# Optimization experiments

Hardware: AMD Instinct MI355X
Metric: run time of the kernel (lower is better)

## Reference

```python
import jax, jax.numpy as jnp
import numpy as np

N_NODES = 20000
N_EDGES = 100000
MUL = 128          # channels per irrep
R = 8              # radial (edge scalar) features
H = 64             # radial MLP hidden width
SILU_NORM = 1.6790390826      # e3nn normalize2mom constant for SiLU
INV_SQRT3 = 1.0 / np.sqrt(3.0)   # wigner-3j values for l<=1 paths
PW_0E = np.sqrt(0.5)   # e3nn path weight: out dim 1, fan-in 2 paths
PW_1O = np.sqrt(1.5)   # e3nn path weight: out dim 3, fan-in 2 paths


def setup_inputs() -> dict:
    key = jax.random.key(0)
    ks = jax.random.split(key, 12)
    return dict(
        node_feats=jax.random.normal(ks[0], (N_NODES, 4 * MUL), jnp.float32),
        edge_attrs=jax.random.normal(ks[1], (N_EDGES, 4), jnp.float32),   # SH: 1x0e+1x1o
        edge_feats=jax.random.normal(ks[2], (N_EDGES, R), jnp.float32),
        edge_index=jax.random.randint(ks[3], (2, N_EDGES), 0, N_NODES),
        W_up_s=jax.random.normal(ks[4], (MUL, MUL), jnp.float32),
        W_up_v=jax.random.normal(ks[5], (MUL, MUL), jnp.float32),
        mlp_w0=jax.random.normal(ks[6], (R, H), jnp.float32),
        mlp_w1=jax.random.normal(ks[7], (H, H), jnp.float32),
        mlp_w2=jax.random.normal(ks[8], (H, H), jnp.float32),
        mlp_w3=jax.random.normal(ks[9], (H, 4 * MUL), jnp.float32),
        W_out_s=jax.random.normal(ks[10], (2 * MUL, MUL), jnp.float32),
        W_out_v=jax.random.normal(ks[11], (2 * MUL, MUL), jnp.float32),
    )


def reference(node_feats, edge_attrs, edge_feats, edge_index,
              W_up_s, W_up_v, mlp_w0, mlp_w1, mlp_w2, mlp_w3,
              W_out_s, W_out_v):
    sender = edge_index[0]
    # split node feats into irrep blocks: 128x0e then 128x1o (channel-major [u, m])
    s = node_feats[:, :MUL]                       # [N, 128]
    v = node_feats[:, MUL:].reshape(-1, MUL, 3)   # [N, 128, 3]
    # linear_up: per-irrep e3nn Linear, fan_in-normalized
    s = (s @ W_up_s) / np.sqrt(MUL)
    v = jnp.einsum('nui,uw->nwi', v, W_up_v) / np.sqrt(MUL)
    # radial MLP -> per-edge tensor-product weights (e3nn FullyConnectedNet)
    act = lambda x: jax.nn.silu(x) * SILU_NORM
    h = act(edge_feats @ (mlp_w0 / np.sqrt(R)))
    h = act(h @ (mlp_w1 / np.sqrt(H)))
    h = act(h @ (mlp_w2 / np.sqrt(H)))
    tpw = h @ (mlp_w3 / np.sqrt(H))               # [E, 4*128]
    w00, w01, w10, w11 = jnp.split(tpw, 4, axis=1)  # instruction order of weight_numel
    # gather sender node features per edge
    ss = s[sender]                                # [E, 128]
    vs = v[sender]                                # [E, 128, 3]
    sh0 = edge_attrs[:, :1]                       # [E, 1]  scalar SH
    sh1 = edge_attrs[:, 1:]                       # [E, 3]  l=1 SH
    # uvu CG tensor product paths (l<=1 wigner-3j)
    a0 = PW_0E * w00 * ss * sh0                                   # 0e x 0e -> 0e
    a1 = (PW_1O * INV_SQRT3) * (w01 * ss)[:, :, None] * sh1[:, None, :]   # 0e x 1o -> 1o
    b1 = (PW_1O * INV_SQRT3) * (w10 * sh0)[:, :, None] * vs              # 1o x 0e -> 1o
    b0 = (PW_0E * INV_SQRT3) * w11 * jnp.einsum('eui,ei->eu', vs, sh1)   # 1o x 1o -> 0e
    # irreps_mid sorted+simplified: 256x0e + 256x1o
    mid_s = jnp.concatenate([a0, b0], axis=1)     # [E, 256]
    mid_v = jnp.concatenate([a1, b1], axis=1)     # [E, 256, 3]
    # final per-irrep linear to target 128x0e + 128x1o
    out_s = (mid_s @ W_out_s) / np.sqrt(2 * MUL)
    out_v = jnp.einsum('eui,uw->ewi', mid_v, W_out_v) / np.sqrt(2 * MUL)
    return jnp.concatenate([out_s, out_v.reshape(out_v.shape[0], 3 * MUL)], axis=1)
```

## Files before the change

kernel.cpp:

```cpp
#include <hip/hip_runtime.h>
#include <stdint.h>

#define N_NODES 20000
#define N_EDGES 100000

typedef __bf16 bf16;
typedef bf16  bf16x8 __attribute__((ext_vector_type(8)));
typedef float f32x4  __attribute__((ext_vector_type(4)));

__device__ __forceinline__ f32x4 mfma16(bf16x8 a, bf16x8 b, f32x4 c) {
  return __builtin_amdgcn_mfma_f32_16x16x32_bf16(a, b, c, 0, 0, 0);
}

__device__ __forceinline__ float silu_(float y) {
  return y / (1.0f + __expf(-y));
}

#define OFF_W0T   0u
#define OFF_W1T   4096u
#define OFF_W2T   12288u
#define OFF_W3T   20480u
#define OFF_WOS   86016u
#define OFF_WOV   151552u
#define OFF_WST   217088u
#define OFF_WVT   249856u
#define OFF_SUP   282624u
#define OFF_VUP   5402624u

__global__ __launch_bounds__(256) void k0_prep(
    const float* __restrict__ wus, const float* __restrict__ wuv,
    const float* __restrict__ w0,  const float* __restrict__ w1,
    const float* __restrict__ w2,  const float* __restrict__ w3,
    const float* __restrict__ wos_g, const float* __restrict__ wov_g,
    char* __restrict__ ws) {
  const int idx = blockIdx.x * 256 + threadIdx.x;
  bf16* W0T = (bf16*)(ws + OFF_W0T);
  bf16* W1T = (bf16*)(ws + OFF_W1T);
  bf16* W2T = (bf16*)(ws + OFF_W2T);
  bf16* W3T = (bf16*)(ws + OFF_W3T);
  bf16* WOS = (bf16*)(ws + OFF_WOS);
  bf16* WOV = (bf16*)(ws + OFF_WOV);
  bf16* WST = (bf16*)(ws + OFF_WST);
  bf16* WVT = (bf16*)(ws + OFF_WVT);

  const float cS   = 0.08838834764831845f;
  const float c0   = 0.35355339059327373f;
  const float c12  = 1.6790390826f / 8.0f;
  const float cosA = 0.04419417382415922f;
  const float cosB = 0.025515518153991442f;
  const float cov  = 0.04419417382415922f;

  if (idx < 16384) {
    int w = idx >> 7, u = idx & 127;
    WST[idx] = (bf16)(wus[u * 128 + w] * cS);
    WVT[idx] = (bf16)(wuv[u * 128 + w] * cS);
  }
  if (idx < 2048) {
    int h = idx >> 5, r = idx & 31;
    W0T[idx] = (bf16)((r < 8) ? w0[r * 64 + h] * c0 : 0.0f);
  }
  if (idx < 4096) {
    int h = idx >> 6, k = idx & 63;
    W1T[idx] = (bf16)(w1[k * 64 + h] * c12);
    W2T[idx] = (bf16)(w2[k * 64 + h] * c12);
  }
  {
    int j = idx >> 6, k = idx & 63;
    W3T[idx] = (bf16)(w3[k * 512 + j] * c12);
    int w = idx >> 8, u = idx & 255;
    WOS[idx] = (bf16)(wos_g[u * 128 + w] * ((u < 128) ? cosA : cosB));
    WOV[idx] = (bf16)(wov_g[u * 128 + w] * cov);
  }
}

__global__ __launch_bounds__(256) void k1_nodeup(const float* __restrict__ nf,
                                                 char* __restrict__ ws) {
  __shared__ bf16 At[64 * 136];
  const int n0 = blockIdx.x * 64;
  const int sid = blockIdx.y;
  const int t = threadIdx.x;

  #pragma unroll
  for (int p = 0; p < 32; p++) {
    int idx = t + p * 256;
    int r = idx >> 7, k = idx & 127;
    int node = n0 + r;
    float v = 0.0f;
    if (node < N_NODES)
      v = (sid == 0) ? nf[node * 512 + k]
                     : nf[node * 512 + 128 + 3 * k + (sid - 1)];
    At[r * 136 + k] = (bf16)v;
  }
  __syncthreads();

  const bf16* BT = (const bf16*)(ws + ((sid == 0) ? OFF_WST : OFF_WVT));
  const int lane = t & 63, wv = t >> 6;
  const int m = lane & 15, q = lane >> 4;
  const int m0 = wv * 16;

  const f32x4 z = {0.f, 0.f, 0.f, 0.f};
  f32x4 acc[8] = {z, z, z, z, z, z, z, z};
  #pragma unroll
  for (int kk = 0; kk < 128; kk += 32) {
    bf16x8 af = *(const bf16x8*)&At[(m0 + m) * 136 + kk + q * 8];
    #pragma unroll
    for (int nt = 0; nt < 8; nt++) {
      bf16x8 bfr = *(const bf16x8*)&BT[(nt * 16 + m) * 128 + kk + q * 8];
      acc[nt] = mfma16(af, bfr, acc[nt]);
    }
  }

  bf16* sup = (bf16*)(ws + OFF_SUP);
  bf16* vup = (bf16*)(ws + OFF_VUP);
  #pragma unroll
  for (int nt = 0; nt < 8; nt++) {
    int col = nt * 16 + m;
    #pragma unroll
    for (int r = 0; r < 4; r++) {
      int row = m0 + q * 4 + r;
      int node = n0 + row;
      if (node < N_NODES) {
        if (sid == 0) sup[node * 128 + col] = (bf16)acc[nt][r];
        else          vup[node * 384 + (sid - 1) * 128 + col] = (bf16)acc[nt][r];
      }
    }
  }
}

__global__ __launch_bounds__(256) void k2_mlp(const float* __restrict__ efeat,
                                              const char* __restrict__ ws,
                                              float* __restrict__ tpw) {
  __shared__ bf16 A0[64 * 40];
  __shared__ bf16 hA[64 * 72];
  __shared__ bf16 hB[64 * 72];
  const int e0 = blockIdx.x * 64;
  const int t = threadIdx.x;
  const int lane = t & 63, wv = t >> 6;
  const int m = lane & 15, q = lane >> 4;
  const int m0 = wv * 16;
  const f32x4 z = {0.f, 0.f, 0.f, 0.f};

  #pragma unroll
  for (int p = 0; p < 8; p++) {
    int idx = t + p * 256;
    int r = idx >> 5, k = idx & 31;
    int e = e0 + r;
    float v = (k < 8 && e < N_EDGES) ? efeat[e * 8 + k] : 0.0f;
    A0[r * 40 + k] = (bf16)v;
  }
  __syncthreads();

  const bf16* W0T = (const bf16*)(ws + OFF_W0T);
  const bf16* W1T = (const bf16*)(ws + OFF_W1T);
  const bf16* W2T = (const bf16*)(ws + OFF_W2T);
  const bf16* W3T = (const bf16*)(ws + OFF_W3T);

  {
    f32x4 acc[4] = {z, z, z, z};
    bf16x8 af = *(const bf16x8*)&A0[(m0 + m) * 40 + q * 8];
    #pragma unroll
    for (int nt = 0; nt < 4; nt++) {
      bf16x8 bfr = *(const bf16x8*)&W0T[(nt * 16 + m) * 32 + q * 8];
      acc[nt] = mfma16(af, bfr, acc[nt]);
    }
    #pragma unroll
    for (int nt = 0; nt < 4; nt++)
      #pragma unroll
      for (int r = 0; r < 4; r++)
        hA[(m0 + q * 4 + r) * 72 + nt * 16 + m] = (bf16)silu_(acc[nt][r]);
  }
  __syncthreads();

  {
    f32x4 acc[4] = {z, z, z, z};
    #pragma unroll
    for (int kk = 0; kk < 64; kk += 32) {
      bf16x8 af = *(const bf16x8*)&hA[(m0 + m) * 72 + kk + q * 8];
      #pragma unroll
      for (int nt = 0; nt < 4; nt++) {
        bf16x8 bfr = *(const bf16x8*)&W1T[(nt * 16 + m) * 64 + kk + q * 8];
        acc[nt] = mfma16(af, bfr, acc[nt]);
      }
    }
    #pragma unroll
    for (int nt = 0; nt < 4; nt++)
      #pragma unroll
      for (int r = 0; r < 4; r++)
        hB[(m0 + q * 4 + r) * 72 + nt * 16 + m] = (bf16)silu_(acc[nt][r]);
  }
  __syncthreads();

  {
    f32x4 acc[4] = {z, z, z, z};
    #pragma unroll
    for (int kk = 0; kk < 64; kk += 32) {
      bf16x8 af = *(const bf16x8*)&hB[(m0 + m) * 72 + kk + q * 8];
      #pragma unroll
      for (int nt = 0; nt < 4; nt++) {
        bf16x8 bfr = *(const bf16x8*)&W2T[(nt * 16 + m) * 64 + kk + q * 8];
        acc[nt] = mfma16(af, bfr, acc[nt]);
      }
    }
    __syncthreads();
    #pragma unroll
    for (int nt = 0; nt < 4; nt++)
      #pragma unroll
      for (int r = 0; r < 4; r++)
        hA[(m0 + q * 4 + r) * 72 + nt * 16 + m] = (bf16)silu_(acc[nt][r]);
  }
  __syncthreads();

  {
    bf16x8 af0 = *(const bf16x8*)&hA[(m0 + m) * 72 + 0  + q * 8];
    bf16x8 af1 = *(const bf16x8*)&hA[(m0 + m) * 72 + 32 + q * 8];
    const int row0 = m0 + q * 4;
    #pragma unroll 4
    for (int nt = 0; nt < 32; nt++) {
      f32x4 acc = z;
      bf16x8 b0 = *(const bf16x8*)&W3T[(nt * 16 + m) * 64 + q * 8];
      bf16x8 b1 = *(const bf16x8*)&W3T[(nt * 16 + m) * 64 + 32 + q * 8];
      acc = mfma16(af0, b0, acc);
      acc = mfma16(af1, b1, acc);
      int col = nt * 16 + m;
      #pragma unroll
      for (int r = 0; r < 4; r++) {
        int e = e0 + row0 + r;
        if (e < N_EDGES) tpw[e * 512 + col] = acc[r];
      }
    }
  }
}

__global__ __launch_bounds__(256) void k3_tp_out(const float* __restrict__ attrs,
                                                 const int* __restrict__ sender,
                                                 const char* __restrict__ ws,
                                                 float* out) {
  __shared__ bf16 A[128 * 72];
  __shared__ int   sLDS[32];
  __shared__ float aLDS[128];
  const int e0 = blockIdx.x * 32;
  const int t = threadIdx.x;
  if (t < 32) sLDS[t] = sender[e0 + t];
  if (t < 128) aLDS[t] = attrs[e0 * 4 + t];
  __syncthreads();

  const bf16* sup = (const bf16*)(ws + OFF_SUP);
  const bf16* vup = (const bf16*)(ws + OFF_VUP);
  const int lane = t & 63, wv = t >> 6;
  const int m = lane & 15, q = lane >> 4;
  const bf16* WB = (const bf16*)(ws + ((wv == 0) ? OFF_WOS : OFF_WOV));

  const int srow = t >> 1;
  const int kh = (t & 1) * 32;
  const bool isS = (srow < 32);
  const int ii = isS ? 0 : ((srow - 32) >> 5);
  const int eL = isS ? srow : ((srow - 32) & 31);
  const int eG = e0 + eL;
  const int se = sLDS[eL];
  const float s0  = aLDS[eL * 4 + 0];
  const float s1x = aLDS[eL * 4 + 1];
  const float s1y = aLDS[eL * 4 + 2];
  const float s1z = aLDS[eL * 4 + 3];
  const float s1i = (ii == 0) ? s1x : ((ii == 1) ? s1y : s1z);
  const float* tpr = out + (size_t)eG * 512;
  const bf16* supR = sup + se * 128;
  const bf16* vupR = vup + se * 384;

  const f32x4 z = {0.f, 0.f, 0.f, 0.f};
  f32x4 acc0[8] = {z, z, z, z, z, z, z, z};
  f32x4 acc1[8] = {z, z, z, z, z, z, z, z};

  for (int kc = 0; kc < 4; kc++) {
    if (kc) __syncthreads();
    if (kc < 2) {
      const int ub = kc * 64 + kh;
      if (isS) {
        #pragma unroll 8
        for (int j = 0; j < 32; j++) {
          int u = ub + j;
          A[srow * 72 + kh + j] = (bf16)(tpr[u] * (float)supR[u] * s0);
        }
      } else {
        #pragma unroll 8
        for (int j = 0; j < 32; j++) {
          int u = ub + j;
          A[srow * 72 + kh + j] = (bf16)(tpr[128 + u] * (float)supR[u] * s1i);
        }
      }
    } else {
      const int ub = (kc - 2) * 64 + kh;
      if (isS) {
        #pragma unroll 8
        for (int j = 0; j < 32; j++) {
          int up = ub + j;
          float dv = (float)vupR[up] * s1x + (float)vupR[128 + up] * s1y +
                     (float)vupR[256 + up] * s1z;
          A[srow * 72 + kh + j] = (bf16)(tpr[384 + up] * dv);
        }
      } else {
        #pragma unroll 8
        for (int j = 0; j < 32; j++) {
          int up = ub + j;
          A[srow * 72 + kh + j] =
              (bf16)(tpr[256 + up] * s0 * (float)vupR[ii * 128 + up]);
        }
      }
    }
    __syncthreads();

    const int kb = kc * 64;
    #pragma unroll
    for (int kk = 0; kk < 64; kk += 32) {
      bf16x8 af0 = *(const bf16x8*)&A[(wv * 32 + m) * 72 + kk + q * 8];
      bf16x8 af1 = *(const bf16x8*)&A[(wv * 32 + 16 + m) * 72 + kk + q * 8];
      #pragma unroll
      for (int nt = 0; nt < 8; nt++) {
        bf16x8 bfr = *(const bf16x8*)&WB[(nt * 16 + m) * 256 + kb + kk + q * 8];
        acc0[nt] = mfma16(af0, bfr, acc0[nt]);
        acc1[nt] = mfma16(af1, bfr, acc1[nt]);
      }
    }
  }

  #pragma unroll
  for (int b = 0; b < 2; b++) {
    const f32x4* accp = b ? acc1 : acc0;
    int rb = wv * 32 + b * 16 + q * 4;
    #pragma unroll
    for (int nt = 0; nt < 8; nt++) {
      int col = nt * 16 + m;
      #pragma unroll
      for (int r = 0; r < 4; r++) {
        int row = rb + r;
        float v = accp[nt][r];
        if (wv == 0) {
          out[(size_t)(e0 + row) * 512 + col] = v;
        } else {
          int i2 = (row - 32) >> 5, eL2 = (row - 32) & 31;
          out[(size_t)(e0 + eL2) * 512 + 128 + 3 * col + i2] = v;
        }
      }
    }
  }
}

extern "C" void kernel_launch(void* const* d_in, const int* in_sizes, int n_in,
                              void* d_out, int out_size, void* d_ws, size_t ws_size,
                              hipStream_t stream) {
  const float* node_feats = (const float*)d_in[0];
  const float* edge_attrs = (const float*)d_in[1];
  const float* edge_feats = (const float*)d_in[2];
  const int*   edge_index = (const int*)d_in[3];
  const float* W_up_s = (const float*)d_in[4];
  const float* W_up_v = (const float*)d_in[5];
  const float* w0 = (const float*)d_in[6];
  const float* w1 = (const float*)d_in[7];
  const float* w2 = (const float*)d_in[8];
  const float* w3 = (const float*)d_in[9];
  const float* Wos = (const float*)d_in[10];
  const float* Wov = (const float*)d_in[11];
  float* out = (float*)d_out;
  char* ws = (char*)d_ws;

  k0_prep<<<dim3(128), dim3(256), 0, stream>>>(W_up_s, W_up_v, w0, w1, w2, w3,
                                               Wos, Wov, ws);
  k1_nodeup<<<dim3(313, 4), dim3(256), 0, stream>>>(node_feats, ws);
  k2_mlp<<<dim3(1563), dim3(256), 0, stream>>>(edge_feats, ws, out);
  k3_tp_out<<<dim3(3125), dim3(256), 0, stream>>>(edge_attrs, edge_index, ws, out);
}
```

Baseline: 542.7 us.

## Fuse radial MLP into tensor-product kernel, keep TP weights in LDS

Merges the radial MLP kernel into the tensor-product/output kernel, so the per-edge 512-wide TP weights stay in shared memory as bf16 instead of being written to and re-read from the output buffer in fp32. The node-up kernel now reads node features once with float4 loads and deinterleaves all four irrep components in one block, rather than launching four strided passes. The TP gather loops are vectorized to 8-wide bf16 loads. The cost is more LDS per block (about 52KB), which limits occupancy, and the MLP work is now split across 32-edge blocks with extra barriers.

```diff
diff --git a/kernel.cpp b/kernel.cpp
--- a/kernel.cpp
+++ b/kernel.cpp
@@ -73,80 +73,107 @@
   }
 }
 
-__global__ __launch_bounds__(256) void k1_nodeup(const float* __restrict__ nf,
-                                                 char* __restrict__ ws) {
-  __shared__ bf16 At[64 * 136];
-  const int n0 = blockIdx.x * 64;
-  const int sid = blockIdx.y;
+__global__ __launch_bounds__(256, 4) void k1_nodeup(const float* __restrict__ nf,
+                                                    char* __restrict__ ws) {
+  __shared__ __align__(16) bf16 tiles[4][32 * 136];
+  const int n0 = blockIdx.x * 32;
   const int t = threadIdx.x;
 
   #pragma unroll
-  for (int p = 0; p < 32; p++) {
-    int idx = t + p * 256;
-    int r = idx >> 7, k = idx & 127;
-    int node = n0 + r;
-    float v = 0.0f;
-    if (node < N_NODES)
-      v = (sid == 0) ? nf[node * 512 + k]
-                     : nf[node * 512 + 128 + 3 * k + (sid - 1)];
-    At[r * 136 + k] = (bf16)v;
-  }
-  __syncthreads();
-
-  const bf16* BT = (const bf16*)(ws + ((sid == 0) ? OFF_WST : OFF_WVT));
-  const int lane = t & 63, wv = t >> 6;
+  for (int p = 0; p < 16; p++) {
+    int idx = p * 256 + t;
+    int r = idx >> 7, c4 = idx & 127;
+    const float4 f = *(const float4*)&nf[(size_t)(n0 + r) * 512 + c4 * 4];
+    float vals[4] = {f.x, f.y, f.z, f.w};
+    #pragma unroll
+    for (int e2 = 0; e2 < 4; e2++) {
+      int g = c4 * 4 + e2;
+      if (g < 128) {
+        tiles[0][r * 136 + g] = (bf16)vals[e2];
+      } else {
+        int gg = g - 128;
+        int u = gg / 3, i = gg - 3 * u;
+        tiles[1 + i][r * 136 + u] = (bf16)vals[e2];
+      }
+    }
+  }
+  __syncthreads();
+
+  const int wv = t >> 6, lane = t & 63;
   const int m = lane & 15, q = lane >> 4;
-  const int m0 = wv * 16;
+  const bf16* BT = (const bf16*)(ws + ((wv == 0) ? OFF_WST : OFF_WVT));
+  const bf16* At = tiles[wv];
 
   const f32x4 z = {0.f, 0.f, 0.f, 0.f};
-  f32x4 acc[8] = {z, z, z, z, z, z, z, z};
+  f32x4 acc[2][8] = {{z, z, z, z, z, z, z, z}, {z, z, z, z, z, z, z, z}};
   #pragma unroll
   for (int kk = 0; kk < 128; kk += 32) {
-    bf16x8 af = *(const bf16x8*)&At[(m0 + m) * 136 + kk + q * 8];
+    bf16x8 af0 = *(const bf16x8*)&At[m * 136 + kk + q * 8];
+    bf16x8 af1 = *(const bf16x8*)&At[(16 + m) * 136 + kk + q * 8];
     #pragma unroll
     for (int nt = 0; nt < 8; nt++) {
       bf16x8 bfr = *(const bf16x8*)&BT[(nt * 16 + m) * 128 + kk + q * 8];
-      acc[nt] = mfma16(af, bfr, acc[nt]);
+      acc[0][nt] = mfma16(af0, bfr, acc[0][nt]);
+      acc[1][nt] = mfma16(af1, bfr, acc[1][nt]);
     }
   }
 
   bf16* sup = (bf16*)(ws + OFF_SUP);
   bf16* vup = (bf16*)(ws + OFF_VUP);
   #pragma unroll
-  for (int nt = 0; nt < 8; nt++) {
-    int col = nt * 16 + m;
-    #pragma unroll
-    for (int r = 0; r < 4; r++) {
-      int row = m0 + q * 4 + r;
-      int node = n0 + row;
-      if (node < N_NODES) {
-        if (sid == 0) sup[node * 128 + col] = (bf16)acc[nt][r];
-        else          vup[node * 384 + (sid - 1) * 128 + col] = (bf16)acc[nt][r];
-      }
-    }
-  }
-}
-
-__global__ __launch_bounds__(256) void k2_mlp(const float* __restrict__ efeat,
-                                              const char* __restrict__ ws,
-                                              float* __restrict__ tpw) {
-  __shared__ bf16 A0[64 * 40];
-  __shared__ bf16 hA[64 * 72];
-  __shared__ bf16 hB[64 * 72];
-  const int e0 = blockIdx.x * 64;
+  for (int rt = 0; rt < 2; rt++) {
+    #pragma unroll
+    for (int nt = 0; nt < 8; nt++) {
+      int col = nt * 16 + m;
+      #pragma unroll
+      for (int r = 0; r < 4; r++) {
+        int node = n0 + rt * 16 + q * 4 + r;
+        if (wv == 0) sup[node * 128 + col] = (bf16)acc[rt][nt][r];
+        else         vup[node * 384 + (wv - 1) * 128 + col] = (bf16)acc[rt][nt][r];
+      }
+    }
+  }
+}
+
+#define SM_TPW 0
+#define SM_A   33280
+#define SM_A0  33280
+#define SM_H0  (33280 + 2560)
+#define SM_H1  (33280 + 7168)
+#define SM_SND 51712
+#define SM_ATT 51840
+#define TPW_LD 520
+
+__global__ __launch_bounds__(256, 3) void k23_fused(
+    const float* __restrict__ efeat, const float* __restrict__ attrs,
+    const int* __restrict__ sender, const char* __restrict__ ws,
+    float* __restrict__ out) {
+  __shared__ __align__(16) char smem[52352];
+  bf16* tpwL = (bf16*)(smem + SM_TPW);
+  bf16* A    = (bf16*)(smem + SM_A);
+  bf16* A0e  = (bf16*)(smem + SM_A0);
+  bf16* h0   = (bf16*)(smem + SM_H0);
+  bf16* h1   = (bf16*)(smem + SM_H1);
+  int*  sLDS = (int*)(smem + SM_SND);
+  float* aLDS = (float*)(smem + SM_ATT);
+
+  const int e0 = blockIdx.x * 32;
   const int t = threadIdx.x;
-  const int lane = t & 63, wv = t >> 6;
+  const int wv = t >> 6, lane = t & 63;
   const int m = lane & 15, q = lane >> 4;
-  const int m0 = wv * 16;
   const f32x4 z = {0.f, 0.f, 0.f, 0.f};
 
-  #pragma unroll
-  for (int p = 0; p < 8; p++) {
-    int idx = t + p * 256;
-    int r = idx >> 5, k = idx & 31;
-    int e = e0 + r;
-    float v = (k < 8 && e < N_EDGES) ? efeat[e * 8 + k] : 0.0f;
-    A0[r * 40 + k] = (bf16)v;
+  {
+    int r = t >> 3, k = t & 7;
+    A0e[r * 40 + k] = (bf16)efeat[(e0 + r) * 8 + k];
+    #pragma unroll
+    for (int pp = 0; pp < 3; pp++) {
+      int pidx = t * 3 + pp;
+      int r2 = pidx / 24, k2 = 8 + pidx % 24;
+      A0e[r2 * 40 + k2] = (bf16)0.0f;
+    }
+    if (t < 32) sLDS[t] = sender[e0 + t];
+    if (t < 128) aLDS[t] = attrs[e0 * 4 + t];
   }
   __syncthreads();
 
@@ -155,99 +182,89 @@
   const bf16* W2T = (const bf16*)(ws + OFF_W2T);
   const bf16* W3T = (const bf16*)(ws + OFF_W3T);
 
-  {
-    f32x4 acc[4] = {z, z, z, z};
-    bf16x8 af = *(const bf16x8*)&A0[(m0 + m) * 40 + q * 8];
-    #pragma unroll
-    for (int nt = 0; nt < 4; nt++) {
-      bf16x8 bfr = *(const bf16x8*)&W0T[(nt * 16 + m) * 32 + q * 8];
-      acc[nt] = mfma16(af, bfr, acc[nt]);
-    }
-    #pragma unroll
-    for (int nt = 0; nt < 4; nt++)
+  const int rt = wv & 1, nh = wv >> 1;
+
+  {
+    f32x4 acc[2] = {z, z};
+    bf16x8 af = *(const bf16x8*)&A0e[(rt * 16 + m) * 40 + q * 8];
+    #pragma unroll
+    for (int ntl = 0; ntl < 2; ntl++) {
+      int ntg = nh * 2 + ntl;
+      bf16x8 bfr = *(const bf16x8*)&W0T[(ntg * 16 + m) * 32 + q * 8];
+      acc[ntl] = mfma16(af, bfr, acc[ntl]);
+    }
+    __syncthreads();
+    #pragma unroll
+    for (int ntl = 0; ntl < 2; ntl++)
       #pragma unroll
       for (int r = 0; r < 4; r++)
-        hA[(m0 + q * 4 + r) * 72 + nt * 16 + m] = (bf16)silu_(acc[nt][r]);
-  }
-  __syncthreads();
-
-  {
-    f32x4 acc[4] = {z, z, z, z};
+        h0[(rt * 16 + q * 4 + r) * 72 + (nh * 2 + ntl) * 16 + m] = (bf16)silu_(acc[ntl][r]);
+  }
+  __syncthreads();
+
+  {
+    f32x4 acc[2] = {z, z};
     #pragma unroll
     for (int kk = 0; kk < 64; kk += 32) {
-      bf16x8 af = *(const bf16x8*)&hA[(m0 + m) * 72 + kk + q * 8];
-      #pragma unroll
-      for (int nt = 0; nt < 4; nt++) {
-        bf16x8 bfr = *(const bf16x8*)&W1T[(nt * 16 + m) * 64 + kk + q * 8];
-        acc[nt] = mfma16(af, bfr, acc[nt]);
-      }
-    }
-    #pragma unroll
-    for (int nt = 0; nt < 4; nt++)
+      bf16x8 af = *(const bf16x8*)&h0[(rt * 16 + m) * 72 + kk + q * 8];
+      #pragma unroll
+      for (int ntl = 0; ntl < 2; ntl++) {
+        int ntg = nh * 2 + ntl;
+        bf16x8 bfr = *(const bf16x8*)&W1T[(ntg * 16 + m) * 64 + kk + q * 8];
+        acc[ntl] = mfma16(af, bfr, acc[ntl]);
+      }
+    }
+    __syncthreads();
+    #pragma unroll
+    for (int ntl = 0; ntl < 2; ntl++)
       #pragma unroll
       for (int r = 0; r < 4; r++)
-        hB[(m0 + q * 4 + r) * 72 + nt * 16 + m] = (bf16)silu_(acc[nt][r]);
-  }
-  __syncthreads();
-
-  {
-    f32x4 acc[4] = {z, z, z, z};
+        h1[(rt * 16 + q * 4 + r) * 72 + (nh * 2 + ntl) * 16 + m] = (bf16)silu_(acc[ntl][r]);
+  }
+  __syncthreads();
+
+  {
+    f32x4 acc[2] = {z, z};
     #pragma unroll
     for (int kk = 0; kk < 64; kk += 32) {
-      bf16x8 af = *(const bf16x8*)&hB[(m0 + m) * 72 + kk + q * 8];
-      #pragma unroll
-      for (int nt = 0; nt < 4; nt++) {
-        bf16x8 bfr = *(const bf16x8*)&W2T[(nt * 16 + m) * 64 + kk + q * 8];
-        acc[nt] = mfma16(af, bfr, acc[nt]);
+      bf16x8 af = *(const bf16x8*)&h1[(rt * 16 + m) * 72 + kk + q * 8];
+      #pragma unroll
+      for (int ntl = 0; ntl < 2; ntl++) {
+        int ntg = nh * 2 + ntl;
+        bf16x8 bfr = *(const bf16x8*)&W2T[(ntg * 16 + m) * 64 + kk + q * 8];
+        acc[ntl] = mfma16(af, bfr, acc[ntl]);
       }
     }
     __syncthreads();
     #pragma unroll
-    for (int nt = 0; nt < 4; nt++)
+    for (int ntl = 0; ntl < 2; ntl++)
       #pragma unroll
       for (int r = 0; r < 4; r++)
-        hA[(m0 + q * 4 + r) * 72 + nt * 16 + m] = (bf16)silu_(acc[nt][r]);
-  }
-  __syncthreads();
-
-  {
-    bf16x8 af0 = *(const bf16x8*)&hA[(m0 + m) * 72 + 0  + q * 8];
-    bf16x8 af1 = *(const bf16x8*)&hA[(m0 + m) * 72 + 32 + q * 8];
-    const int row0 = m0 + q * 4;
+        h0[(rt * 16 + q * 4 + r) * 72 + (nh * 2 + ntl) * 16 + m] = (bf16)silu_(acc[ntl][r]);
+  }
+  __syncthreads();
+
+  {
+    bf16x8 af0 = *(const bf16x8*)&h0[(rt * 16 + m) * 72 + 0  + q * 8];
+    bf16x8 af1 = *(const bf16x8*)&h0[(rt * 16 + m) * 72 + 32 + q * 8];
     #pragma unroll 4
-    for (int nt = 0; nt < 32; nt++) {
+    for (int i = 0; i < 16; i++) {
+      int ntg = nh * 16 + i;
       f32x4 acc = z;
-      bf16x8 b0 = *(const bf16x8*)&W3T[(nt * 16 + m) * 64 + q * 8];
-      bf16x8 b1 = *(const bf16x8*)&W3T[(nt * 16 + m) * 64 + 32 + q * 8];
+      bf16x8 b0 = *(const bf16x8*)&W3T[(ntg * 16 + m) * 64 + q * 8];
+      bf16x8 b1 = *(const bf16x8*)&W3T[(ntg * 16 + m) * 64 + 32 + q * 8];
       acc = mfma16(af0, b0, acc);
       acc = mfma16(af1, b1, acc);
-      int col = nt * 16 + m;
-      #pragma unroll
-      for (int r = 0; r < 4; r++) {
-        int e = e0 + row0 + r;
-        if (e < N_EDGES) tpw[e * 512 + col] = acc[r];
-      }
-    }
-  }
-}
-
-__global__ __launch_bounds__(256) void k3_tp_out(const float* __restrict__ attrs,
-                                                 const int* __restrict__ sender,
-                                                 const char* __restrict__ ws,
-                                                 float* out) {
-  __shared__ bf16 A[128 * 72];
-  __shared__ int   sLDS[32];
-  __shared__ float aLDS[128];
-  const int e0 = blockIdx.x * 32;
-  const int t = threadIdx.x;
-  if (t < 32) sLDS[t] = sender[e0 + t];
-  if (t < 128) aLDS[t] = attrs[e0 * 4 + t];
+      int col = ntg * 16 + m;
+      #pragma unroll
+      for (int r = 0; r < 4; r++)
+        tpwL[(rt * 16 + q * 4 + r) * TPW_LD + col] = (bf16)acc[r];
+    }
+  }
   __syncthreads();
 
   const bf16* sup = (const bf16*)(ws + OFF_SUP);
   const bf16* vup = (const bf16*)(ws + OFF_VUP);
-  const int lane = t & 63, wv = t >> 6;
-  const int m = lane & 15, q = lane >> 4;
   const bf16* WB = (const bf16*)(ws + ((wv == 0) ? OFF_WOS : OFF_WOV));
 
   const int srow = t >> 1;
@@ -255,18 +272,16 @@
   const bool isS = (srow < 32);
   const int ii = isS ? 0 : ((srow - 32) >> 5);
   const int eL = isS ? srow : ((srow - 32) & 31);
-  const int eG = e0 + eL;
   const int se = sLDS[eL];
   const float s0  = aLDS[eL * 4 + 0];
   const float s1x = aLDS[eL * 4 + 1];
   const float s1y = aLDS[eL * 4 + 2];
   const float s1z = aLDS[eL * 4 + 3];
   const float s1i = (ii == 0) ? s1x : ((ii == 1) ? s1y : s1z);
-  const float* tpr = out + (size_t)eG * 512;
+  const bf16* tpr = tpwL + eL * TPW_LD;
   const bf16* supR = sup + se * 128;
   const bf16* vupR = vup + se * 384;
 
-  const f32x4 z = {0.f, 0.f, 0.f, 0.f};
   f32x4 acc0[8] = {z, z, z, z, z, z, z, z};
   f32x4 acc1[8] = {z, z, z, z, z, z, z, z};
 
@@ -275,34 +290,55 @@
     if (kc < 2) {
       const int ub = kc * 64 + kh;
       if (isS) {
-        #pragma unroll 8
-        for (int j = 0; j < 32; j++) {
-          int u = ub + j;
-          A[srow * 72 + kh + j] = (bf16)(tpr[u] * (float)supR[u] * s0);
+        #pragma unroll
+        for (int j0 = 0; j0 < 32; j0 += 8) {
+          bf16x8 tv = *(const bf16x8*)&tpr[ub + j0];
+          bf16x8 sv = *(const bf16x8*)&supR[ub + j0];
+          bf16x8 o;
+          #pragma unroll
+          for (int e = 0; e < 8; e++)
+            o[e] = (bf16)((float)tv[e] * (float)sv[e] * s0);
+          *(bf16x8*)&A[srow * 72 + kh + j0] = o;
         }
       } else {
-        #pragma unroll 8
-        for (int j = 0; j < 32; j++) {
-          int u = ub + j;
-          A[srow * 72 + kh + j] = (bf16)(tpr[128 + u] * (float)supR[u] * s1i);
+        #pragma unroll
+        for (int j0 = 0; j0 < 32; j0 += 8) {
+          bf16x8 tv = *(const bf16x8*)&tpr[128 + ub + j0];
+          bf16x8 sv = *(const bf16x8*)&supR[ub + j0];
+          bf16x8 o;
+          #pragma unroll
+          for (int e = 0; e < 8; e++)
+            o[e] = (bf16)((float)tv[e] * (float)sv[e] * s1i);
+          *(bf16x8*)&A[srow * 72 + kh + j0] = o;
         }
       }
     } else {
       const int ub = (kc - 2) * 64 + kh;
       if (isS) {
-        #pragma unroll 8
-        for (int j = 0; j < 32; j++) {
-          int up = ub + j;
-          float dv = (float)vupR[up] * s1x + (float)vupR[128 + up] * s1y +
-                     (float)vupR[256 + up] * s1z;
-          A[srow * 72 + kh + j] = (bf16)(tpr[384 + up] * dv);
+        #pragma unroll
+        for (int j0 = 0; j0 < 32; j0 += 8) {
+          bf16x8 tv = *(const bf16x8*)&tpr[384 + ub + j0];
+          bf16x8 vx = *(const bf16x8*)&vupR[ub + j0];
+          bf16x8 vy = *(const bf16x8*)&vupR[128 + ub + j0];
+          bf16x8 vz = *(const bf16x8*)&vupR[256 + ub + j0];
+          bf16x8 o;
+          #pragma unroll
+          for (int e = 0; e < 8; e++) {
+            float dv = (float)vx[e] * s1x + (float)vy[e] * s1y + (float)vz[e] * s1z;
+            o[e] = (bf16)((float)tv[e] * dv);
+          }
+          *(bf16x8*)&A[srow * 72 + kh + j0] = o;
         }
       } else {
-        #pragma unroll 8
-        for (int j = 0; j < 32; j++) {
-          int up = ub + j;
-          A[srow * 72 + kh + j] =
-              (bf16)(tpr[256 + up] * s0 * (float)vupR[ii * 128 + up]);
+        #pragma unroll
+        for (int j0 = 0; j0 < 32; j0 += 8) {
+          bf16x8 tv = *(const bf16x8*)&tpr[256 + ub + j0];
+          bf16x8 vv = *(const bf16x8*)&vupR[ii * 128 + ub + j0];
+          bf16x8 o;
+          #pragma unroll
+          for (int e = 0; e < 8; e++)
+            o[e] = (bf16)((float)tv[e] * s0 * (float)vv[e]);
+          *(bf16x8*)&A[srow * 72 + kh + j0] = o;
         }
       }
     }
@@ -364,7 +400,7 @@
 
   k0_prep<<<dim3(128), dim3(256), 0, stream>>>(W_up_s, W_up_v, w0, w1, w2, w3,
                                                Wos, Wov, ws);
-  k1_nodeup<<<dim3(313, 4), dim3(256), 0, stream>>>(node_feats, ws);
-  k2_mlp<<<dim3(1563), dim3(256), 0, stream>>>(edge_feats, ws, out);
-  k3_tp_out<<<dim3(3125), dim3(256), 0, stream>>>(edge_attrs, edge_index, ws, out);
-}
+  k1_nodeup<<<dim3(625), dim3(256), 0, stream>>>(node_feats, ws);
+  k23_fused<<<dim3(3125), dim3(256), 0, stream>>>(edge_feats, edge_attrs,
+                                                  edge_index, ws, out);
+}
```

Measured after the change: 460.6 us. 1.18x faster.
